# Kernel tuning notes

Measured on AMD Instinct MI355X. Metric: run time of the kernel, lower is better.

Reference implementation:

```python
import jax, jax.numpy as jnp
import numpy as np

B, NB, H, E, NCT, NL = 16, 4096, 128, 65536, 32, 2
LN_EPS = 1e-5


def _layernorm(x, scale, bias):
    mu = jnp.mean(x, axis=-1, keepdims=True)
    var = jnp.var(x, axis=-1, keepdims=True)
    return (x - mu) / jnp.sqrt(var + LN_EPS) * scale + bias


def setup_inputs() -> dict:
    key = jax.random.key(0)
    ks = jax.random.split(key, 18)
    s = 1.0 / np.sqrt(H)
    inp = {
        'block_tokens': jax.random.normal(ks[0], (B, NB, H), jnp.float32),
        'edge_structure': jnp.full((E,), 0.5, jnp.float32),
        'ct_emb': 0.1 * jax.random.normal(ks[1], (NCT, E), jnp.float32),
        'W_proj': s * jax.random.normal(ks[2], (H, H), jnp.float32),
        'b_proj': jnp.zeros((H,), jnp.float32),
        'W_gate': (1.0 / np.sqrt(2 * H)) * jax.random.normal(ks[3], (2 * H, H), jnp.float32),
        'b_gate': jnp.zeros((H,), jnp.float32),
        'ln_scale': jnp.ones((NL, H), jnp.float32),
        'ln_bias': jnp.zeros((NL, H), jnp.float32),
        'W1': s * jax.random.normal(ks[4], (NL, H, 2 * H), jnp.float32),
        'b1': jnp.zeros((NL, 2 * H), jnp.float32),
        'W2': (1.0 / np.sqrt(2 * H)) * jax.random.normal(ks[5], (NL, 2 * H, H), jnp.float32),
        'b2': jnp.zeros((NL, H), jnp.float32),
        'cancer_type': jax.random.randint(ks[6], (B,), 0, NCT),
        'edge_src': jax.random.randint(ks[7], (E,), 0, NB),
        'edge_dst': jax.random.randint(ks[8], (E,), 0, NB),
        'block_active': jax.random.bernoulli(ks[9], 0.9, (B, NB)),
    }
    return inp


def reference(block_tokens, edge_structure, ct_emb, W_proj, b_proj, W_gate, b_gate,
              ln_scale, ln_bias, W1, b1, W2, b2,
              cancer_type, edge_src, edge_dst, block_active):
    # per-edge signed weights, masked by active src/dst blocks  -> (B, E)
    structure = jax.nn.sigmoid(edge_structure)
    edge_w = structure[None, :] * ct_emb[cancer_type]
    edge_w = edge_w * block_active[:, edge_src].astype(edge_w.dtype) \
                    * block_active[:, edge_dst].astype(edge_w.dtype)
    # route projection + ELU
    h_route = jax.nn.elu(jnp.einsum('bnh,hd->bnd', block_tokens, W_proj) + b_proj)
    # gather sources, weight, scatter-add to destinations
    weighted = edge_w[..., None] * h_route[:, edge_src, :]          # (B, E, H)
    messages = jnp.zeros_like(block_tokens).at[:, edge_dst, :].add(weighted)
    # gated residual
    gate = jax.nn.sigmoid(
        jnp.einsum('bnh,hd->bnd', jnp.concatenate([block_tokens, messages], axis=-1), W_gate) + b_gate)
    x = block_tokens + gate * messages
    # norm + FFN layers (dropout is identity at inference)
    for l in range(NL):
        normed = _layernorm(x, ln_scale[l], ln_bias[l])
        h = jax.nn.elu(jnp.einsum('bnh,hf->bnf', normed, W1[l]) + b1[l])
        x = x + jnp.einsum('bnf,fh->bnh', h, W2[l]) + b2[l]
    return (x, edge_w)
```

## Files before the change

kernel.cpp:

```cpp
#include <hip/hip_runtime.h>
#include <hip/hip_bf16.h>

#define BB     16
#define NBLK   4096
#define HD     128
#define NE     65536
#define MTOT   (BB * NBLK)

typedef __attribute__((ext_vector_type(8))) short bf16x8;
typedef __attribute__((ext_vector_type(4))) float f32x4;

__device__ __forceinline__ float bf2f(unsigned short u) {
    union { unsigned int i; float f; } v; v.i = ((unsigned int)u) << 16; return v.f;
}
__device__ __forceinline__ unsigned short f2bf(float f) {
    union { float f; unsigned int i; } v; v.f = f;
    unsigned int u = v.i;
    unsigned int r = u + 0x7FFFu + ((u >> 16) & 1u);
    return (unsigned short)(r >> 16);
}
__device__ __forceinline__ float ldf(const void* p, size_t i, int f32m) {
    return f32m ? ((const float*)p)[i] : bf2f(((const unsigned short*)p)[i]);
}
__device__ __forceinline__ int get_active(const void* p, int i, int mode) {
    switch (mode) {
        case 1:  return ((const unsigned char*)p)[i] != 0;
        case 2:  return ((const unsigned short*)p)[i] != 0;
        case 3:  return ((const float*)p)[i] != 0.f;
        default: return ((const int*)p)[i] != 0;
    }
}
__device__ __forceinline__ float elu_f(float v) {
    const float e = __expf(v);
    return v > 0.f ? v : e - 1.f;
}
__device__ __forceinline__ float sig_f(float v) {
    return 1.f / (1.f + __expf(-v));
}

__global__ void probe_k(const unsigned int* __restrict__ es,
                        const unsigned int* __restrict__ act,
                        int* __restrict__ flags)
{
    const int lane = threadIdx.x;
    const unsigned int v0 = act[lane], v1 = act[64 + lane];
    auto le1  = [](unsigned int v) { return v <= 1u; };
    auto byt  = [](unsigned int v) {
        return ((v & 0xFFu) <= 1u) && (((v >> 8) & 0xFFu) <= 1u) &&
               (((v >> 16) & 0xFFu) <= 1u) && ((v >> 24) <= 1u); };
    auto f32b = [](unsigned int v) { return v == 0u || v == 0x3F800000u; };
    auto bfb  = [](unsigned int v) {
        unsigned short h0 = (unsigned short)(v & 0xFFFFu), h1 = (unsigned short)(v >> 16);
        return (h0 == 0u || h0 == 0x3F80u) && (h1 == 0u || h1 == 0x3F80u); };
    const unsigned long long m_le1 = __ballot(le1(v0) && le1(v1));
    const unsigned long long m_byt = __ballot(byt(v0) && byt(v1));
    const unsigned long long m_f32 = __ballot(f32b(v0) && f32b(v1));
    const unsigned long long m_bf  = __ballot(bfb(v0) && bfb(v1));
    if (lane == 0) {
        flags[0] = (es[0] != 0x3F003F00u) ? 1 : 0;
        const unsigned long long full = ~0ull;
        flags[1] = (m_le1 == full) ? 0
                 : (m_byt == full) ? 1
                 : (m_f32 == full) ? 3
                 : (m_bf  == full) ? 2 : 0;
    }
}

__global__ __launch_bounds__(256) void cvt_k(const void* __restrict__ bt,
                                             unsigned short* __restrict__ bt16,
                                             const int* __restrict__ flags)
{
    const size_t i = ((size_t)blockIdx.x * 256 + threadIdx.x) * 8;
    if (flags[0]) {
        const float* q = (const float*)bt + i;
        f32x4 lo = *(const f32x4*)q;
        f32x4 hi = *(const f32x4*)(q + 4);
        bf16x8 r;
        #pragma unroll
        for (int j = 0; j < 4; ++j) { r[j] = (short)f2bf(lo[j]); r[4 + j] = (short)f2bf(hi[j]); }
        *(bf16x8*)(bt16 + i) = r;
    } else {
        *(bf16x8*)(bt16 + i) = *(const bf16x8*)((const unsigned short*)bt + i);
    }
}

__global__ __launch_bounds__(256) void transpose_k(
    const void* p0, const void* p1, const void* p2, const void* p3,
    const void* p4, const void* p5, unsigned short* __restrict__ wsT,
    const int* __restrict__ flags)
{
    const void* srcs[6]  = {p0, p1, p2, p3, p4, p5};
    const int eoffs[6]   = {0, 0, 0, 32768, 0, 32768};
    const int Ks[6]      = {128, 256, 128, 128, 256, 256};
    const int nsh[6]     = {7,   7,   8,   8,   7,   7};
    const int offs[6]    = {0, 16384, 49152, 81920, 114688, 147456};
    const int f32m = flags[0];
    const int z = blockIdx.y;
    const int K = Ks[z];
    const int Nn = 1 << nsh[z];
    const int idx = blockIdx.x * 256 + threadIdx.x;
    if (idx >= K * Nn) return;
    const int k = idx >> nsh[z];
    const int n = idx & (Nn - 1);
    wsT[offs[z] + n * K + k] = f2bf(ldf(srcs[z], (size_t)eoffs[z] + idx, f32m));
}

__global__ __launch_bounds__(256) void csr_count_k(const int* __restrict__ edst,
                                                   int* __restrict__ cnt)
{
    const int e = blockIdx.x * 256 + threadIdx.x;
    atomicAdd(&cnt[edst[e]], 1);
}

__global__ __launch_bounds__(1024) void csr_scan_k(const int* __restrict__ cnt,
                                                   int* __restrict__ ofs,
                                                   int* __restrict__ cur)
{
    __shared__ int part[1024];
    const int t = threadIdx.x;
    const int4 c = ((const int4*)cnt)[t];
    part[t] = c.x + c.y + c.z + c.w;
    __syncthreads();
    #pragma unroll
    for (int off = 1; off < 1024; off <<= 1) {
        const int v = (t >= off) ? part[t - off] : 0;
        __syncthreads();
        part[t] += v;
        __syncthreads();
    }
    const int base = t ? part[t - 1] : 0;
    int4 o;
    o.x = base; o.y = o.x + c.x; o.z = o.y + c.y; o.w = o.z + c.z;
    ((int4*)ofs)[t] = o;
    ((int4*)cur)[t] = o;
    if (t == 1023) ofs[4096] = part[1023];
}

__global__ __launch_bounds__(256) void csr_fill_k(const int* __restrict__ edst,
                                                  int* __restrict__ cur,
                                                  int* __restrict__ eidx,
                                                  int* __restrict__ pos_e)
{
    const int e = blockIdx.x * 256 + threadIdx.x;
    const int pos = atomicAdd(&cur[edst[e]], 1);
    eidx[pos] = e;
    pos_e[e] = pos;
}

__global__ __launch_bounds__(256) void edge_k(
    const void* __restrict__ es, const void* __restrict__ ctE,
    const int* __restrict__ ctype, const int* __restrict__ esrc, const int* __restrict__ edst,
    const void* __restrict__ act, const int* __restrict__ pos_e,
    float* __restrict__ out_ew, float2* __restrict__ compact,
    const int* __restrict__ flags)
{
    const int f32m = flags[0], am = flags[1];
    const int idx = blockIdx.x * 256 + threadIdx.x;
    const int b = idx >> 16;
    const int e = idx & 65535;
    const int s = esrc[e];
    const float sv  = sig_f(ldf(es, e, f32m));
    const float emb = ldf(ctE, (size_t)ctype[b] * NE + e, f32m);
    const int a1 = get_active(act, b * NBLK + s, am);
    const int a2 = get_active(act, b * NBLK + edst[e], am);
    const float w = (a1 && a2) ? sv * emb : 0.f;
    out_ew[idx] = w;
    compact[((size_t)b << 16) + pos_e[e]] = make_float2(w, __int_as_float(s));
}

__global__ __launch_bounds__(256) void gather_k(
    const float2* __restrict__ compact, const int* __restrict__ ofs,
    const unsigned short* __restrict__ hr, unsigned short* __restrict__ msg)
{
    const int blk = blockIdx.x;
    const int xcd = blk & 7;
    const int i   = blk >> 3;
    const int b   = xcd * 2 + (i & 1);
    const int d   = ((i >> 1) << 2) | (threadIdx.x >> 6);
    const int lane = threadIdx.x & 63;
    const int sub  = lane >> 4;
    const int l15  = lane & 15;
    const int j1 = ofs[d + 1];
    const size_t bbase = (size_t)b * NBLK * HD;
    const float2* cb = compact + ((size_t)b << 16);
    float acc[8];
    #pragma unroll
    for (int i2 = 0; i2 < 8; ++i2) acc[i2] = 0.f;
    int j = ofs[d] + sub;
    float2 c = (j < j1) ? cb[j] : make_float2(0.f, 0.f);
    while (j < j1) {
        const int jn = j + 4;
        const float2 cn = (jn < j1) ? cb[jn] : make_float2(0.f, 0.f);
        if (c.x != 0.f) {
            const int src = __float_as_int(c.y);
            const bf16x8 v = *(const bf16x8*)(hr + bbase + (size_t)src * HD + l15 * 8);
            #pragma unroll
            for (int i2 = 0; i2 < 8; ++i2)
                acc[i2] += c.x * bf2f((unsigned short)v[i2]);
        }
        c = cn; j = jn;
    }
    #pragma unroll
    for (int i2 = 0; i2 < 8; ++i2) {
        acc[i2] += __shfl_xor(acc[i2], 16);
        acc[i2] += __shfl_xor(acc[i2], 32);
    }
    if (sub == 0) {
        bf16x8 o;
        #pragma unroll
        for (int i2 = 0; i2 < 8; ++i2) o[i2] = (short)f2bf(acc[i2]);
        *(bf16x8*)(msg + bbase + (size_t)d * HD + l15 * 8) = o;
    }
}

template<int K, int N, int EPI>
__global__ __launch_bounds__(256) void gemm_k(
    const unsigned short* __restrict__ A,
    const unsigned short* __restrict__ WT,
    const void* __restrict__ bias, long boff,
    unsigned short* __restrict__ outb,
    const int* __restrict__ flags)
{
    constexpr int KI    = K / 32;
    constexpr int NCW   = N / 4;
    constexpr int NTW   = NCW / 16;
    constexpr int TILES = 8;
    constexpr int NBUF  = (K == 128 ? 4 : 2);
    const int f32m = flags[0];
    const int t    = threadIdx.x;
    const int lane = t & 63;
    const int wave = t >> 6;
    const int q    = lane >> 4;
    const int l15  = lane & 15;
    const int n0   = wave * NCW;

    bf16x8 Bf[KI][NTW];
    #pragma unroll
    for (int ki = 0; ki < KI; ++ki)
        #pragma unroll
        for (int nt = 0; nt < NTW; ++nt)
            Bf[ki][nt] = *(const bf16x8*)(WT + (size_t)(n0 + nt * 16 + l15) * K + ki * 32 + q * 8);

    float biasv[NTW];
    #pragma unroll
    for (int nt = 0; nt < NTW; ++nt)
        biasv[nt] = ldf(bias, boff + n0 + nt * 16 + l15, f32m);

    const int tile0 = blockIdx.x * TILES;
    bf16x8 Af[NBUF][KI];
    auto loadA = [&](int tt) {
        const int arow = (tile0 + tt) * 16 + l15;
        #pragma unroll
        for (int ki = 0; ki < KI; ++ki)
            Af[tt % NBUF][ki] = *(const bf16x8*)(A + (size_t)arow * K + ki * 32 + q * 8);
    };
    #pragma unroll
    for (int p = 0; p < NBUF; ++p) loadA(p);

    #pragma unroll
    for (int tt = 0; tt < TILES; ++tt) {
        const int s = tt % NBUF;
        f32x4 acc[NTW];
        #pragma unroll
        for (int i = 0; i < NTW; ++i) acc[i] = (f32x4){0.f, 0.f, 0.f, 0.f};
        #pragma unroll
        for (int ki = 0; ki < KI; ++ki)
            #pragma unroll
            for (int nt = 0; nt < NTW; ++nt)
                acc[nt] = __builtin_amdgcn_mfma_f32_16x16x32_bf16(Af[s][ki], Bf[ki][nt], acc[nt], 0, 0, 0);

        if (tt + NBUF < TILES) loadA(tt + NBUF);

        const int m0 = (tile0 + tt) * 16;
        #pragma unroll
        for (int nt = 0; nt < NTW; ++nt) {
            #pragma unroll
            for (int r = 0; r < 4; ++r) {
                const int row = m0 + q * 4 + r;
                const int col = n0 + nt * 16 + l15;
                const float v = acc[nt][r] + biasv[nt];
                outb[(size_t)row * N + col] = f2bf(elu_f(v));
            }
        }
    }
}

#define XI(xt, row, col)      x_lds[xt][row][((col) + 4 * (row)) & 127]
#define UI(hf, tl, row, col)  U[hf][tl][row][((col) + 8 * (row)) & 255]

__global__ __launch_bounds__(512, 2) void mega_k(
    const unsigned short* __restrict__ bt16,
    const unsigned short* __restrict__ msg,
    const void* __restrict__ btf,
    const unsigned short* __restrict__ WT,
    const void* __restrict__ bg,
    const void* __restrict__ b1, const void* __restrict__ b2,
    const void* __restrict__ lns, const void* __restrict__ lnb,
    float* __restrict__ xout,
    const int* __restrict__ flags)
{
    __shared__ __align__(16) float          x_lds[4][32][128];
    __shared__ __align__(16) unsigned short U[2][2][32][256];

    const int f32m = flags[0];
    const int t    = threadIdx.x;
    const int lane = t & 63;
    const int wave = t >> 6;
    const int hf   = wave >> 2;
    const int wv   = wave & 3;
    const int q    = lane >> 4;
    const int l15  = lane & 15;
    const int rhf  = blockIdx.x * 128 + hf * 64;
    const int ng   = wv * 32;

    float          btv[2][2][2][4];
    unsigned short mgu[2][2][2][4];
    #pragma unroll
    for (int tl = 0; tl < 2; ++tl)
        #pragma unroll
        for (int tt = 0; tt < 2; ++tt)
            #pragma unroll
            for (int nt = 0; nt < 2; ++nt)
                #pragma unroll
                for (int r = 0; r < 4; ++r) {
                    const size_t gi = (size_t)(rhf + tl * 32 + tt * 16 + q * 4 + r) * HD
                                      + ng + nt * 16 + l15;
                    btv[tl][tt][nt][r] = ldf(btf, gi, f32m);
                    mgu[tl][tt][nt][r] = msg[gi];
                }

    const unsigned short* WgT = WT + 16384;

    bf16x8 Bg[8][2];
    #pragma unroll
    for (int ki = 0; ki < 8; ++ki)
        #pragma unroll
        for (int nt = 0; nt < 2; ++nt)
            Bg[ki][nt] = *(const bf16x8*)(WgT + (size_t)(ng + nt * 16 + l15) * 256 + ki * 32 + q * 8);
    float biasg[2];
    #pragma unroll
    for (int nt = 0; nt < 2; ++nt) biasg[nt] = ldf(bg, ng + nt * 16 + l15, f32m);

    #pragma unroll
    for (int tl = 0; tl < 2; ++tl) {
        const int xt = hf * 2 + tl;
        bf16x8 Ag[2][8];
        #pragma unroll
        for (int tt = 0; tt < 2; ++tt) {
            const int arow = rhf + tl * 32 + tt * 16 + l15;
            #pragma unroll
            for (int ki = 0; ki < 8; ++ki) {
                const int k = ki * 32 + q * 8;
                Ag[tt][ki] = (k < HD)
                    ? *(const bf16x8*)(bt16 + (size_t)arow * HD + k)
                    : *(const bf16x8*)(msg  + (size_t)arow * HD + (k - HD));
            }
        }
        #pragma unroll
        for (int tt = 0; tt < 2; ++tt) {
            f32x4 acc[2];
            #pragma unroll
            for (int nt = 0; nt < 2; ++nt) acc[nt] = (f32x4){0.f, 0.f, 0.f, 0.f};
            __builtin_amdgcn_s_setprio(1);
            #pragma unroll
            for (int ki = 0; ki < 8; ++ki)
                #pragma unroll
                for (int nt = 0; nt < 2; ++nt)
                    acc[nt] = __builtin_amdgcn_mfma_f32_16x16x32_bf16(Ag[tt][ki], Bg[ki][nt], acc[nt], 0, 0, 0);
            __builtin_amdgcn_s_setprio(0);
            #pragma unroll
            for (int nt = 0; nt < 2; ++nt)
                #pragma unroll
                for (int r = 0; r < 4; ++r) {
                    const float g = sig_f(acc[nt][r] + biasg[nt]);
                    XI(xt, tt * 16 + q * 4 + r, ng + nt * 16 + l15) =
                        btv[tl][tt][nt][r] + g * bf2f(mgu[tl][tt][nt][r]);
                }
        }
    }
    __syncthreads();

    const int rowln = (t & 255) >> 3;
    const int seg   = t & 7;
    const int n1 = wv * 64;
    const int n2 = wv * 32;

    #pragma unroll
    for (int l = 0; l < 2; ++l) {
        const unsigned short* W1T = WT + (l ? 81920  : 49152);
        const unsigned short* W2T = WT + (l ? 147456 : 114688);
        const long b1o = l ? 256 : 0, b2o = l ? 128 : 0, lno = l ? 128 : 0;

        bf16x8 B1[4][4];
        #pragma unroll
        for (int ki = 0; ki < 4; ++ki)
            #pragma unroll
            for (int nt = 0; nt < 4; ++nt)
                B1[ki][nt] = *(const bf16x8*)(W1T + (size_t)(n1 + nt * 16 + l15) * 128 + ki * 32 + q * 8);
        float bias1[4];
        #pragma unroll
        for (int nt = 0; nt < 4; ++nt) bias1[nt] = ldf(b1, b1o + n1 + nt * 16 + l15, f32m);

        float lsv[16], lbv[16];
        #pragma unroll
        for (int j = 0; j < 4; ++j)
            #pragma unroll
            for (int k = 0; k < 4; ++k) {
                const int col = seg * 16 + j * 4 + k;
                lsv[j * 4 + k] = ldf(lns, lno + col, f32m);
                lbv[j * 4 + k] = ldf(lnb, lno + col, f32m);
            }

        #pragma unroll
        for (int tl = 0; tl < 2; ++tl) {
            const int xt = hf * 2 + tl;
            f32x4 xv[4];
            #pragma unroll
            for (int j = 0; j < 4; ++j)
                xv[j] = *(const f32x4*)&XI(xt, rowln, seg * 16 + j * 4);
            float s = 0.f, ss = 0.f;
            #pragma unroll
            for (int j = 0; j < 4; ++j)
                #pragma unroll
                for (int k = 0; k < 4; ++k) { const float v = xv[j][k]; s += v; ss += v * v; }
            #pragma unroll
            for (int off = 1; off < 8; off <<= 1) { s += __shfl_xor(s, off); ss += __shfl_xor(ss, off); }
            const float mu = s * (1.f / 128.f);
            const float rs = rsqrtf(ss * (1.f / 128.f) - mu * mu + 1e-5f);
            bf16x8 nv[2];
            #pragma unroll
            for (int j = 0; j < 4; ++j)
                #pragma unroll
                for (int k = 0; k < 4; ++k) {
                    const float nn = (xv[j][k] - mu) * rs * lsv[j * 4 + k] + lbv[j * 4 + k];
                    nv[j >> 1][(j & 1) * 4 + k] = (short)f2bf(nn);
                }
            *(bf16x8*)&UI(hf, tl, rowln, seg * 16)     = nv[0];
            *(bf16x8*)&UI(hf, tl, rowln, seg * 16 + 8) = nv[1];
        }
        __syncthreads();

        bf16x8 An[2][2][4];
        #pragma unroll
        for (int tl = 0; tl < 2; ++tl)
            #pragma unroll
            for (int tt = 0; tt < 2; ++tt)
                #pragma unroll
                for (int ki = 0; ki < 4; ++ki)
                    An[tl][tt][ki] = *(const bf16x8*)&UI(hf, tl, tt * 16 + l15, ki * 32 + q * 8);
        __syncthreads();

        #pragma unroll
        for (int tl = 0; tl < 2; ++tl)
            #pragma unroll
            for (int tt = 0; tt < 2; ++tt) {
                f32x4 acc[4];
                #pragma unroll
                for (int nt = 0; nt < 4; ++nt) acc[nt] = (f32x4){0.f, 0.f, 0.f, 0.f};
                __builtin_amdgcn_s_setprio(1);
                #pragma unroll
                for (int ki = 0; ki < 4; ++ki)
                    #pragma unroll
                    for (int nt = 0; nt < 4; ++nt)
                        acc[nt] = __builtin_amdgcn_mfma_f32_16x16x32_bf16(An[tl][tt][ki], B1[ki][nt], acc[nt], 0, 0, 0);
                __builtin_amdgcn_s_setprio(0);
                #pragma unroll
                for (int nt = 0; nt < 4; ++nt)
                    #pragma unroll
                    for (int r = 0; r < 4; ++r)
                        UI(hf, tl, tt * 16 + q * 4 + r, n1 + nt * 16 + l15) =
                            f2bf(elu_f(acc[nt][r] + bias1[nt]));
            }

        bf16x8 B2[8][2];
        #pragma unroll
        for (int ki = 0; ki < 8; ++ki)
            #pragma unroll
            for (int nt = 0; nt < 2; ++nt)
                B2[ki][nt] = *(const bf16x8*)(W2T + (size_t)(n2 + nt * 16 + l15) * 256 + ki * 32 + q * 8);
        float bias2[2];
        #pragma unroll
        for (int nt = 0; nt < 2; ++nt) bias2[nt] = ldf(b2, b2o + n2 + nt * 16 + l15, f32m);
        __syncthreads();

        #pragma unroll
        for (int tl = 0; tl < 2; ++tl) {
            const int xt = hf * 2 + tl;
            #pragma unroll
            for (int tt = 0; tt < 2; ++tt) {
                bf16x8 Ah[8];
                #pragma unroll
                for (int ki = 0; ki < 8; ++ki)
                    Ah[ki] = *(const bf16x8*)&UI(hf, tl, tt * 16 + l15, ki * 32 + q * 8);
                f32x4 acc[2];
                #pragma unroll
                for (int nt = 0; nt < 2; ++nt) acc[nt] = (f32x4){0.f, 0.f, 0.f, 0.f};
                __builtin_amdgcn_s_setprio(1);
                #pragma unroll
                for (int ki = 0; ki < 8; ++ki)
                    #pragma unroll
                    for (int nt = 0; nt < 2; ++nt)
                        acc[nt] = __builtin_amdgcn_mfma_f32_16x16x32_bf16(Ah[ki], B2[ki][nt], acc[nt], 0, 0, 0);
                __builtin_amdgcn_s_setprio(0);
                #pragma unroll
                for (int nt = 0; nt < 2; ++nt)
                    #pragma unroll
                    for (int r = 0; r < 4; ++r)
                        XI(xt, tt * 16 + q * 4 + r, n2 + nt * 16 + l15) += acc[nt][r] + bias2[nt];
            }
        }
        __syncthreads();
    }

    #pragma unroll
    for (int xt = 0; xt < 4; ++xt) {
        float* xo = xout + (size_t)(blockIdx.x * 128 + xt * 32) * HD;
        #pragma unroll
        for (int j = 0; j < 2; ++j) {
            const int idx = j * 512 + t;
            const int r2  = idx >> 5;
            const int c4  = (idx & 31) * 4;
            *(f32x4*)(xo + (size_t)idx * 4) = *(const f32x4*)&XI(xt, r2, c4);
        }
    }
}

extern "C" void kernel_launch(void* const* d_in, const int* in_sizes, int n_in,
                              void* d_out, int out_size, void* d_ws, size_t ws_size,
                              hipStream_t stream)
{
    (void)in_sizes; (void)n_in; (void)out_size; (void)ws_size;

    const void* bt  = d_in[0];
    const void* es  = d_in[1];
    const void* ctE = d_in[2];
    const void* Wp  = d_in[3];
    const void* bp  = d_in[4];
    const void* Wg  = d_in[5];
    const void* bg  = d_in[6];
    const void* lns = d_in[7];
    const void* lnb = d_in[8];
    const void* W1  = d_in[9];
    const void* b1  = d_in[10];
    const void* W2  = d_in[11];
    const void* b2  = d_in[12];
    const int* ctype = (const int*)d_in[13];
    const int* esrc  = (const int*)d_in[14];
    const int* edst  = (const int*)d_in[15];
    const void* act  = d_in[16];

    float* out_x  = (float*)d_out;
    float* out_ew = out_x + (size_t)MTOT * HD;
    float* x = out_x;

    char* ws = (char*)d_ws;
    int*            flags = (int*)ws;
    unsigned short* msg   = (unsigned short*)(ws + 1024);
    unsigned short* bt16  = (unsigned short*)(ws + 1024 + (16ull << 20));
    unsigned short* hr    = (unsigned short*)(ws + 1024 + (32ull << 20));
    char* base48 = ws + 1024 + (48ull << 20);
    int*            cnt     = (int*)(base48);
    int*            ofs     = (int*)(base48 + (16 << 10));
    int*            cur     = (int*)(base48 + (36 << 10));
    int*            eidx    = (int*)(base48 + (52 << 10));
    int*            pos_e   = (int*)(base48 + (308 << 10));
    unsigned short* WT      = (unsigned short*)(base48 + (576 << 10));
    float2*         compact = (float2*)(base48 + (1 << 20));

    const int M = MTOT;

    probe_k<<<1, 64, 0, stream>>>((const unsigned int*)es, (const unsigned int*)act, flags);
    hipMemsetAsync(cnt, 0, NBLK * sizeof(int), stream);

    cvt_k<<<dim3((M * HD / 8) / 256), 256, 0, stream>>>(bt, bt16, flags);
    transpose_k<<<dim3(128, 6), 256, 0, stream>>>(Wp, Wg, W1, W1, W2, W2, WT, flags);

    csr_count_k<<<dim3(NE / 256), 256, 0, stream>>>(edst, cnt);
    csr_scan_k<<<dim3(1), 1024, 0, stream>>>(cnt, ofs, cur);
    csr_fill_k<<<dim3(NE / 256), 256, 0, stream>>>(edst, cur, eidx, pos_e);

    edge_k<<<dim3((BB * NE) / 256), 256, 0, stream>>>(
        es, ctE, ctype, esrc, edst, act, pos_e, out_ew, compact, flags);

    gemm_k<128, 128, 0><<<dim3(M / 128), 256, 0, stream>>>(
        bt16, WT + 0, bp, 0, hr, flags);

    gather_k<<<dim3(M / 4), 256, 0, stream>>>(compact, ofs, hr, msg);

    mega_k<<<dim3(M / 128), 512, 0, stream>>>(
        bt16, msg, bt, WT, bg, b1, b2, lns, lnb, x, flags);
}
```

Before: 294.5 us.

## Fuse fp32-to-bf16 conversion into route projection GEMM and prefetch layer-1 weights

```diff
diff --git a/kernel.cpp b/kernel.cpp
--- a/kernel.cpp
+++ b/kernel.cpp
@@ -14,10 +14,10 @@
     union { unsigned int i; float f; } v; v.i = ((unsigned int)u) << 16; return v.f;
 }
 __device__ __forceinline__ unsigned short f2bf(float f) {
-    union { float f; unsigned int i; } v; v.f = f;
-    unsigned int u = v.i;
-    unsigned int r = u + 0x7FFFu + ((u >> 16) & 1u);
-    return (unsigned short)(r >> 16);
+    __bf16 h = (__bf16)f;
+    unsigned short u;
+    __builtin_memcpy(&u, &h, 2);
+    return u;
 }
 __device__ __forceinline__ float ldf(const void* p, size_t i, int f32m) {
     return f32m ? ((const float*)p)[i] : bf2f(((const unsigned short*)p)[i]);
@@ -66,24 +66,6 @@
     }
 }
 
-__global__ __launch_bounds__(256) void cvt_k(const void* __restrict__ bt,
-                                             unsigned short* __restrict__ bt16,
-                                             const int* __restrict__ flags)
-{
-    const size_t i = ((size_t)blockIdx.x * 256 + threadIdx.x) * 8;
-    if (flags[0]) {
-        const float* q = (const float*)bt + i;
-        f32x4 lo = *(const f32x4*)q;
-        f32x4 hi = *(const f32x4*)(q + 4);
-        bf16x8 r;
-        #pragma unroll
-        for (int j = 0; j < 4; ++j) { r[j] = (short)f2bf(lo[j]); r[4 + j] = (short)f2bf(hi[j]); }
-        *(bf16x8*)(bt16 + i) = r;
-    } else {
-        *(bf16x8*)(bt16 + i) = *(const bf16x8*)((const unsigned short*)bt + i);
-    }
-}
-
 __global__ __launch_bounds__(256) void transpose_k(
     const void* p0, const void* p1, const void* p2, const void* p3,
     const void* p4, const void* p5, unsigned short* __restrict__ wsT,
@@ -213,26 +195,41 @@
     }
 }
 
-template<int K, int N, int EPI>
-__global__ __launch_bounds__(256) void gemm_k(
-    const unsigned short* __restrict__ A,
+__global__ __launch_bounds__(256) void route_k(
+    const void* __restrict__ bt,
+    unsigned short* __restrict__ bt16,
     const unsigned short* __restrict__ WT,
-    const void* __restrict__ bias, long boff,
-    unsigned short* __restrict__ outb,
+    const void* __restrict__ bias,
+    unsigned short* __restrict__ hr,
     const int* __restrict__ flags)
 {
-    constexpr int KI    = K / 32;
-    constexpr int NCW   = N / 4;
-    constexpr int NTW   = NCW / 16;
-    constexpr int TILES = 8;
-    constexpr int NBUF  = (K == 128 ? 4 : 2);
+    constexpr int K = 128, N = 128, KI = 4, NTW = 2, TILES = 8, NBUF = 4;
     const int f32m = flags[0];
     const int t    = threadIdx.x;
     const int lane = t & 63;
     const int wave = t >> 6;
     const int q    = lane >> 4;
     const int l15  = lane & 15;
-    const int n0   = wave * NCW;
+    const int n0   = wave * 32;
+
+    {
+        const size_t base = (size_t)blockIdx.x * (128 * HD);
+        #pragma unroll
+        for (int it = 0; it < 8; ++it) {
+            const size_t i = base + (size_t)it * 2048 + (size_t)t * 8;
+            if (f32m) {
+                const float* qp = (const float*)bt + i;
+                f32x4 lo = *(const f32x4*)qp;
+                f32x4 hi = *(const f32x4*)(qp + 4);
+                bf16x8 r;
+                #pragma unroll
+                for (int j = 0; j < 4; ++j) { r[j] = (short)f2bf(lo[j]); r[4 + j] = (short)f2bf(hi[j]); }
+                *(bf16x8*)(bt16 + i) = r;
+            } else {
+                *(bf16x8*)(bt16 + i) = *(const bf16x8*)((const unsigned short*)bt + i);
+            }
+        }
+    }
 
     bf16x8 Bf[KI][NTW];
     #pragma unroll
@@ -240,19 +237,33 @@
         #pragma unroll
         for (int nt = 0; nt < NTW; ++nt)
             Bf[ki][nt] = *(const bf16x8*)(WT + (size_t)(n0 + nt * 16 + l15) * K + ki * 32 + q * 8);
-
     float biasv[NTW];
     #pragma unroll
     for (int nt = 0; nt < NTW; ++nt)
-        biasv[nt] = ldf(bias, boff + n0 + nt * 16 + l15, f32m);
+        biasv[nt] = ldf(bias, n0 + nt * 16 + l15, f32m);
 
     const int tile0 = blockIdx.x * TILES;
     bf16x8 Af[NBUF][KI];
     auto loadA = [&](int tt) {
         const int arow = (tile0 + tt) * 16 + l15;
-        #pragma unroll
-        for (int ki = 0; ki < KI; ++ki)
-            Af[tt % NBUF][ki] = *(const bf16x8*)(A + (size_t)arow * K + ki * 32 + q * 8);
+        if (f32m) {
+            const float* ap = (const float*)bt + (size_t)arow * K;
+            #pragma unroll
+            for (int ki = 0; ki < KI; ++ki) {
+                const int k = ki * 32 + q * 8;
+                f32x4 a0 = *(const f32x4*)(ap + k);
+                f32x4 a1 = *(const f32x4*)(ap + k + 4);
+                bf16x8 r;
+                #pragma unroll
+                for (int j = 0; j < 4; ++j) { r[j] = (short)f2bf(a0[j]); r[4 + j] = (short)f2bf(a1[j]); }
+                Af[tt % NBUF][ki] = r;
+            }
+        } else {
+            const unsigned short* ap = (const unsigned short*)bt + (size_t)arow * K;
+            #pragma unroll
+            for (int ki = 0; ki < KI; ++ki)
+                Af[tt % NBUF][ki] = *(const bf16x8*)(ap + ki * 32 + q * 8);
+        }
     };
     #pragma unroll
     for (int p = 0; p < NBUF; ++p) loadA(p);
@@ -279,7 +290,7 @@
                 const int row = m0 + q * 4 + r;
                 const int col = n0 + nt * 16 + l15;
                 const float v = acc[nt][r] + biasv[nt];
-                outb[(size_t)row * N + col] = f2bf(elu_f(v));
+                hr[(size_t)row * N + col] = f2bf(elu_f(v));
             }
         }
     }
@@ -312,6 +323,10 @@
     const int l15  = lane & 15;
     const int rhf  = blockIdx.x * 128 + hf * 64;
     const int ng   = wv * 32;
+    const int n1   = wv * 64;
+    const int n2   = wv * 32;
+    const int rowln = (t & 255) >> 3;
+    const int seg   = t & 7;
 
     float          btv[2][2][2][4];
     unsigned short mgu[2][2][2][4];
@@ -378,28 +393,25 @@
                 }
         }
     }
-    __syncthreads();
-
-    const int rowln = (t & 255) >> 3;
-    const int seg   = t & 7;
-    const int n1 = wv * 64;
-    const int n2 = wv * 32;
-
-    #pragma unroll
-    for (int l = 0; l < 2; ++l) {
-        const unsigned short* W1T = WT + (l ? 81920  : 49152);
-        const unsigned short* W2T = WT + (l ? 147456 : 114688);
-        const long b1o = l ? 256 : 0, b2o = l ? 128 : 0, lno = l ? 128 : 0;
-
-        bf16x8 B1[4][4];
+
+    bf16x8 B1[4][4];
+    float  bias1[4];
+    auto loadB1 = [&](const unsigned short* W1T, long b1o) {
         #pragma unroll
         for (int ki = 0; ki < 4; ++ki)
             #pragma unroll
             for (int nt = 0; nt < 4; ++nt)
                 B1[ki][nt] = *(const bf16x8*)(W1T + (size_t)(n1 + nt * 16 + l15) * 128 + ki * 32 + q * 8);
-        float bias1[4];
         #pragma unroll
         for (int nt = 0; nt < 4; ++nt) bias1[nt] = ldf(b1, b1o + n1 + nt * 16 + l15, f32m);
+    };
+    loadB1(WT + 49152, 0);
+    __syncthreads();
+
+    #pragma unroll
+    for (int l = 0; l < 2; ++l) {
+        const unsigned short* W2T = WT + (l ? 147456 : 114688);
+        const long b2o = l ? 128 : 0, lno = l ? 128 : 0;
 
         float lsv[16], lbv[16];
         #pragma unroll
@@ -509,6 +521,8 @@
                         XI(xt, tt * 16 + q * 4 + r, n2 + nt * 16 + l15) += acc[nt][r] + bias2[nt];
             }
         }
+
+        if (l == 0) loadB1(WT + 81920, 256);
         __syncthreads();
     }
 
@@ -572,8 +586,9 @@
     probe_k<<<1, 64, 0, stream>>>((const unsigned int*)es, (const unsigned int*)act, flags);
     hipMemsetAsync(cnt, 0, NBLK * sizeof(int), stream);
 
-    cvt_k<<<dim3((M * HD / 8) / 256), 256, 0, stream>>>(bt, bt16, flags);
     transpose_k<<<dim3(128, 6), 256, 0, stream>>>(Wp, Wg, W1, W1, W2, W2, WT, flags);
+
+    route_k<<<dim3(M / 128), 256, 0, stream>>>(bt, bt16, WT + 0, bp, hr, flags);
 
     csr_count_k<<<dim3(NE / 256), 256, 0, stream>>>(edst, cnt);
     csr_scan_k<<<dim3(1), 1024, 0, stream>>>(cnt, ofs, cur);
@@ -582,9 +597,6 @@
     edge_k<<<dim3((BB * NE) / 256), 256, 0, stream>>>(
         es, ctE, ctype, esrc, edst, act, pos_e, out_ew, compact, flags);
 
-    gemm_k<128, 128, 0><<<dim3(M / 128), 256, 0, stream>>>(
-        bt16, WT + 0, bp, 0, hr, flags);
-
     gather_k<<<dim3(M / 4), 256, 0, stream>>>(compact, ofs, hr, msg);
 
     mega_k<<<dim3(M / 128), 512, 0, stream>>>(
```

After: 296.1 us. No clear change (+0.5%).
